# Kernel optimization log

Measured on AMD Instinct MI355X. Metric: run time of the kernel, lower is better.

## Reference

```python
import jax, jax.numpy as jnp
import numpy as np

N, NFEAT, NHID1, NHID2, NCLASS, ATT_H = 6000, 512, 64, 64, 8, 16
ALPHA = 0.2
NEG_INF = -9e15


def _xavier(key, shape, gain=1.414):
    fan_in, fan_out = shape[0], shape[1]
    a = gain * np.sqrt(6.0 / (fan_in + fan_out))
    return jax.random.uniform(key, shape, jnp.float32, -a, a)


def setup_inputs() -> dict:
    key = jax.random.key(0)
    ks = jax.random.split(key, 24)
    inp = {
        'x': jax.random.normal(ks[0], (N, NFEAT), jnp.float32),
        'sadj': jax.random.randint(ks[1], (N, N), 0, 2, jnp.int32),
        'fadj': jax.random.randint(ks[2], (N, N), 0, 2, jnp.int32),
    }
    i = 3
    for pfx in ('s1', 's2', 'c'):
        inp[pfx + '_w1'] = _xavier(ks[i], (NFEAT, NHID1)); i += 1
        inp[pfx + '_a1'] = _xavier(ks[i], (2 * NHID1, 1)); i += 1
        inp[pfx + '_w2'] = _xavier(ks[i], (NHID1, NHID2)); i += 1
        inp[pfx + '_a2'] = _xavier(ks[i], (2 * NHID2, 1)); i += 1
    inp['att_w1'] = _xavier(ks[i], (NHID2, ATT_H), 1.0); i += 1
    inp['att_b1'] = jnp.zeros((ATT_H,), jnp.float32)
    inp['att_w2'] = _xavier(ks[i], (ATT_H, 1), 1.0); i += 1
    inp['mlp_w'] = _xavier(ks[i], (NHID2, NCLASS), 1.0); i += 1
    inp['mlp_b'] = jnp.zeros((NCLASS,), jnp.float32)
    return inp


def gat_layer(h, adj, w, a, concat):
    # h: [N, F_in], adj: [N, N] (0/1), w: [F_in, F_out], a: [2*F_out, 1]
    d = w.shape[1]
    Wh = h @ w                               # [N, F_out]
    e = (Wh @ a[:d]) + (Wh @ a[d:]).T        # [N,1] + [1,N] -> [N,N]
    e = jax.nn.leaky_relu(e, ALPHA)
    att = jnp.where(adj > 0, e, NEG_INF)
    att = jax.nn.softmax(att, axis=1)        # masked row softmax (dropout=0 in eval)
    h_prime = att @ Wh                       # [N, F_out]
    return jax.nn.elu(h_prime) if concat else h_prime


def gat_net(x, adj, w1, a1, w2, a2):
    # nheads=1: single head concat == head output
    h = gat_layer(x, adj, w1, a1, concat=True)
    h = jax.nn.elu(gat_layer(h, adj, w2, a2, concat=False))
    return jax.nn.log_softmax(h, axis=1)


def reference(x, sadj, fadj,
              s1_w1, s1_a1, s1_w2, s1_a2,
              s2_w1, s2_a1, s2_w2, s2_a2,
              c_w1, c_a1, c_w2, c_a2,
              att_w1, att_b1, att_w2, mlp_w, mlp_b):
    emb1 = gat_net(x, sadj, s1_w1, s1_a1, s1_w2, s1_a2)
    com1 = gat_net(x, sadj, c_w1, c_a1, c_w2, c_a2)
    com2 = gat_net(x, fadj, c_w1, c_a1, c_w2, c_a2)
    emb2 = gat_net(x, fadj, s2_w1, s2_a1, s2_w2, s2_a2)
    Xcom = (com1 + com2) / 2
    z = jnp.stack([emb1, emb2, Xcom], axis=1)        # [N, 3, nhid2]
    w = jnp.tanh(z @ att_w1 + att_b1) @ att_w2       # [N, 3, 1]
    beta = jax.nn.softmax(w, axis=1)
    emb = (beta * z).sum(axis=1)                     # [N, nhid2]
    output = jax.nn.log_softmax(emb @ mlp_w + mlp_b, axis=1)
    return (output, beta, emb1, com1, com2, emb2, emb)
```

## Files before the change

kernel.cpp:

```cpp
#include <hip/hip_runtime.h>
#include <cstdint>
#include <cstddef>

#define NN 6000
#define WPR 96
#define NWORDS 94
#define LOG2E 1.4426950408889634f

#define OFF_OUTPUT 0
#define OFF_BETA   48000
#define OFF_EMB1   66000
#define OFF_COM1   450000
#define OFF_COM2   834000
#define OFF_EMB2   1218000
#define OFF_EMB    1602000

typedef unsigned long long u64;
typedef unsigned int uint;
typedef unsigned short ushort;

typedef __bf16 bf16x8 __attribute__((ext_vector_type(8)));
typedef float f32x4 __attribute__((ext_vector_type(4)));
typedef ushort u16x8 __attribute__((ext_vector_type(8)));

__device__ __forceinline__ float wsum64(float v) {
#pragma unroll
  for (int off = 32; off > 0; off >>= 1) v += __shfl_xor(v, off);
  return v;
}

__device__ __forceinline__ ushort bf16rne(float x) {
  uint b = __float_as_uint(x);
  uint r = b + 0x7FFFu + ((b >> 16) & 1u);
  return (ushort)(r >> 16);
}
__device__ __forceinline__ float bf16tof(ushort h) {
  return __uint_as_float((uint)h << 16);
}

__global__ __launch_bounds__(256) void pack_kernel(const int* __restrict__ sadj,
                                                   const int* __restrict__ fadj,
                                                   u64* __restrict__ sbits,
                                                   u64* __restrict__ fbits) {
  const int lane = threadIdx.x & 63;
  const int wid = (blockIdx.x * 256 + threadIdx.x) >> 6;
  const int nw = (gridDim.x * 256) >> 6;
  const int per_mat = NN * WPR;
  for (int t = wid; t < 2 * per_mat; t += nw) {
    int m = t / per_mat;
    int rem = t - m * per_mat;
    int row = rem / WPR;
    int wi = rem - row * WPR;
    const int* adj = m ? fadj : sadj;
    int j = wi * 64 + lane;
    int pred = 0;
    if (j < NN) pred = (adj[(size_t)row * NN + j] != 0);
    u64 mask = __ballot(pred);
    if (lane == 0) (m ? fbits : sbits)[row * WPR + wi] = mask;
  }
}

struct GemmArgs { const float* X; const float* W; const float* A; float* wh; float* f; float* g; };
struct GemmArgs4 { GemmArgs a[4]; };

__global__ __launch_bounds__(256) void gemm_fg_kernel(GemmArgs4 P, int K) {
  GemmArgs A = P.a[blockIdx.y];
  const int w = threadIdx.x >> 6, lane = threadIdx.x & 63;
  const int r0 = blockIdx.x * 16 + w * 4;
  float acc[4] = {0.f, 0.f, 0.f, 0.f};
  const float* X0 = A.X + (size_t)r0 * K;
  for (int k = 0; k < K; k += 4) {
    float xa[4][4];
    *(float4*)xa[0] = *(const float4*)(X0 + k);
    *(float4*)xa[1] = *(const float4*)(X0 + K + k);
    *(float4*)xa[2] = *(const float4*)(X0 + 2 * (size_t)K + k);
    *(float4*)xa[3] = *(const float4*)(X0 + 3 * (size_t)K + k);
#pragma unroll
    for (int kk = 0; kk < 4; ++kk) {
      float wv = A.W[(size_t)(k + kk) * 64 + lane];
#pragma unroll
      for (int r = 0; r < 4; ++r) acc[r] = fmaf(xa[r][kk], wv, acc[r]);
    }
  }
  float af = A.A[lane], ag = A.A[64 + lane];
#pragma unroll
  for (int r = 0; r < 4; ++r) {
    A.wh[(size_t)(r0 + r) * 64 + lane] = acc[r];
    float pf = wsum64(acc[r] * af);
    float pg = wsum64(acc[r] * ag);
    if (lane == 0) { A.f[r0 + r] = pf * LOG2E; A.g[r0 + r] = pg * LOG2E; }
  }
}

struct TransArgs { const float* wh; ushort* bhi; ushort* blo; };
struct TransArgs4 { TransArgs a[4]; };

__global__ __launch_bounds__(256) void trans_kernel(TransArgs4 P) {
  TransArgs A = P.a[blockIdx.y];
  const int jt = blockIdx.x;
  __shared__ float t[64][69];
  const int tid = threadIdx.x;
#pragma unroll
  for (int it = 0; it < 4; ++it) {
    int jl = (tid >> 4) + it * 16;
    int j = jt * 64 + jl;
    float4 v = make_float4(0.f, 0.f, 0.f, 0.f);
    if (j < NN) v = *(const float4*)(A.wh + (size_t)j * 64 + (tid & 15) * 4);
    int d0 = (tid & 15) * 4;
    t[jl][d0] = v.x; t[jl][d0 + 1] = v.y; t[jl][d0 + 2] = v.z; t[jl][d0 + 3] = v.w;
  }
  __syncthreads();
  const int w = tid >> 6, lane = tid & 63, q = lane >> 4, m16 = lane & 15;
#pragma unroll
  for (int fi0 = 0; fi0 < 2; ++fi0) {
    int fi = w + fi0 * 4;
    int k0 = fi >> 2, n0 = fi & 3;
    u16x8 hv, lv;
#pragma unroll
    for (int i = 0; i < 8; ++i) {
      float x = t[k0 * 32 + q * 8 + i][n0 * 16 + m16];
      ushort h = bf16rne(x);
      hv[i] = h;
      lv[i] = bf16rne(x - bf16tof(h));
    }
    size_t off = ((size_t)jt * 8 + fi) * 64 + lane;
    *(u16x8*)(A.bhi + off * 8) = hv;
    *(u16x8*)(A.blo + off * 8) = lv;
  }
}

struct Agg2Args { const u64* bits; const float* f; const float* g;
                  const ushort* bhi; const ushort* blo; float* out; };
struct Agg2Args4 { Agg2Args a[4]; };

template <int MODE>
__global__ __launch_bounds__(512) void agg2_kernel(Agg2Args4 P) {
  const int bid = blockIdx.x;
  const int combo = (bid & 7) >> 1;
  const int mt = ((bid >> 3) << 1) | (bid & 1);
  Agg2Args A = P.a[combo];
  const int w = threadIdx.x >> 6, lane = threadIdx.x & 63;
  const int rg = w & 3, jh = w >> 2;
  const int q = lane >> 4, m16 = lane & 15;
  const int row = mt * 64 + rg * 16 + m16;
  const int rc = row < NN ? row : NN - 1;
  const float fr = A.f[rc];
  const u64* brow = A.bits + (size_t)rc * WPR;

  f32x4 acc[4] = {{0,0,0,0},{0,0,0,0},{0,0,0,0},{0,0,0,0}};
  float sp = 0.f;

  for (int jt = jh; jt < NWORDS; jt += 2) {
    u64 word = brow[jt];
    u16x8 ph[2], pl[2];
#pragma unroll
    for (int k0 = 0; k0 < 2; ++k0) {
      uint byt = (uint)(word >> (k0 * 32 + q * 8)) & 0xFFu;
      const float* gp = A.g + jt * 64 + k0 * 32 + q * 8;
      float4 gA = *(const float4*)gp;
      float4 gB = *(const float4*)(gp + 4);
      float ge[8] = {gA.x, gA.y, gA.z, gA.w, gB.x, gB.y, gB.z, gB.w};
      u16x8 hv, lv;
#pragma unroll
      for (int i = 0; i < 8; ++i) {
        float e = fr + ge[i];
        float lr = fmaxf(e, 0.2f * e);
        float p = exp2f(lr);
        p = (byt & (1u << i)) ? p : 0.f;
        sp += p;
        ushort h = bf16rne(p);
        hv[i] = h;
        lv[i] = bf16rne(p - bf16tof(h));
      }
      ph[k0] = hv; pl[k0] = lv;
    }
    const u16x8* BH = (const u16x8*)A.bhi + ((size_t)jt * 8) * 64 + lane;
    const u16x8* BL = (const u16x8*)A.blo + ((size_t)jt * 8) * 64 + lane;
    bf16x8 a0h = __builtin_bit_cast(bf16x8, ph[0]);
    bf16x8 a1h = __builtin_bit_cast(bf16x8, ph[1]);
    bf16x8 a0l = __builtin_bit_cast(bf16x8, pl[0]);
    bf16x8 a1l = __builtin_bit_cast(bf16x8, pl[1]);
#pragma unroll
    for (int n0 = 0; n0 < 4; ++n0) {
      u16x8 bh0 = BH[n0 * 64], bh1 = BH[(4 + n0) * 64];
      u16x8 bl0 = BL[n0 * 64], bl1 = BL[(4 + n0) * 64];
      bf16x8 b0h = __builtin_bit_cast(bf16x8, bh0);
      bf16x8 b1h = __builtin_bit_cast(bf16x8, bh1);
      bf16x8 b0l = __builtin_bit_cast(bf16x8, bl0);
      bf16x8 b1l = __builtin_bit_cast(bf16x8, bl1);
      acc[n0] = __builtin_amdgcn_mfma_f32_16x16x32_bf16(a0h, b0h, acc[n0], 0, 0, 0);
      acc[n0] = __builtin_amdgcn_mfma_f32_16x16x32_bf16(a1h, b1h, acc[n0], 0, 0, 0);
      acc[n0] = __builtin_amdgcn_mfma_f32_16x16x32_bf16(a0h, b0l, acc[n0], 0, 0, 0);
      acc[n0] = __builtin_amdgcn_mfma_f32_16x16x32_bf16(a1h, b1l, acc[n0], 0, 0, 0);
      acc[n0] = __builtin_amdgcn_mfma_f32_16x16x32_bf16(a0l, b0h, acc[n0], 0, 0, 0);
      acc[n0] = __builtin_amdgcn_mfma_f32_16x16x32_bf16(a1l, b1h, acc[n0], 0, 0, 0);
    }
  }

  sp += __shfl_xor(sp, 16);
  sp += __shfl_xor(sp, 32);

  __shared__ float cb[64][68];
  __shared__ float spb[64];
  if (jh == 0) {
#pragma unroll
    for (int n0 = 0; n0 < 4; ++n0)
#pragma unroll
      for (int r = 0; r < 4; ++r)
        cb[rg * 16 + q * 4 + r][n0 * 16 + m16] = acc[n0][r];
    if (lane < 16) spb[rg * 16 + lane] = sp;
  }
  __syncthreads();
  if (jh == 1) {
    if (lane < 16) spb[rg * 16 + lane] += sp;
  }
  __syncthreads();
  if (jh == 1) {
    float ot[4][4];
#pragma unroll
    for (int r = 0; r < 4; ++r) {
      float sprow = spb[rg * 16 + q * 4 + r];
#pragma unroll
      for (int n0 = 0; n0 < 4; ++n0) {
        float o = acc[n0][r] + cb[rg * 16 + q * 4 + r][n0 * 16 + m16];
        o /= sprow;
        ot[n0][r] = (o > 0.f) ? o : expm1f(o);
      }
    }
#pragma unroll
    for (int r = 0; r < 4; ++r) {
      int orow = mt * 64 + rg * 16 + q * 4 + r;
      float v0 = ot[0][r], v1 = ot[1][r], v2 = ot[2][r], v3 = ot[3][r];
      if (MODE == 1) {
        float mx = fmaxf(fmaxf(v0, v1), fmaxf(v2, v3));
#pragma unroll
        for (int off = 1; off < 16; off <<= 1) mx = fmaxf(mx, __shfl_xor(mx, off));
        float se = __expf(v0 - mx) + __expf(v1 - mx) + __expf(v2 - mx) + __expf(v3 - mx);
#pragma unroll
        for (int off = 1; off < 16; off <<= 1) se += __shfl_xor(se, off);
        float lse = mx + logf(se);
        v0 -= lse; v1 -= lse; v2 -= lse; v3 -= lse;
      }
      if (orow < NN) {
        float* op = A.out + (size_t)orow * 64 + m16;
        op[0] = v0; op[16] = v1; op[32] = v2; op[48] = v3;
      }
    }
  }
}

__global__ __launch_bounds__(256) void fuse_kernel(float* __restrict__ out,
                                                   const float* __restrict__ aw1,
                                                   const float* __restrict__ ab1,
                                                   const float* __restrict__ aw2,
                                                   const float* __restrict__ mlpw,
                                                   const float* __restrict__ mlpb) {
  __shared__ float zs[4][64];
  const int w = threadIdx.x >> 6, lane = threadIdx.x & 63;
  const int i = blockIdx.x * 4 + w;

  const float* emb1 = out + OFF_EMB1;
  const float* com1 = out + OFF_COM1;
  const float* com2 = out + OFF_COM2;
  const float* emb2 = out + OFF_EMB2;

  float z0 = emb1[(size_t)i * 64 + lane];
  float z1 = emb2[(size_t)i * 64 + lane];
  float z2 = 0.5f * (com1[(size_t)i * 64 + lane] + com2[(size_t)i * 64 + lane]);
  float zk[3] = {z0, z1, z2};
  float wk[3];
#pragma unroll
  for (int k = 0; k < 3; ++k) {
    zs[w][lane] = zk[k];
    int h = lane & 15;
    float dot = ab1[h];
    for (int d = 0; d < 64; ++d) dot = fmaf(zs[w][d], aw1[d * 16 + h], dot);
    float c = tanhf(dot) * aw2[h];
#pragma unroll
    for (int off = 1; off < 16; off <<= 1) c += __shfl_xor(c, off);
    wk[k] = c;
  }
  float mw = fmaxf(wk[0], fmaxf(wk[1], wk[2]));
  float e0 = __expf(wk[0] - mw), e1 = __expf(wk[1] - mw), e2 = __expf(wk[2] - mw);
  float s = e0 + e1 + e2;
  float b0 = e0 / s, b1 = e1 / s, b2 = e2 / s;
  float emb = b0 * z0 + b1 * z1 + b2 * z2;
  out[OFF_EMB + (size_t)i * 64 + lane] = emb;
  if (lane == 0) {
    float* bp = out + OFF_BETA + (size_t)i * 3;
    bp[0] = b0; bp[1] = b1; bp[2] = b2;
  }
  zs[w][lane] = emb;
  int c8 = lane & 7;
  float lg = mlpb[c8];
  for (int d = 0; d < 64; ++d) lg = fmaf(zs[w][d], mlpw[d * 8 + c8], lg);
  float mx = lg;
#pragma unroll
  for (int off = 1; off < 8; off <<= 1) mx = fmaxf(mx, __shfl_xor(mx, off));
  float ex = __expf(lg - mx);
  float se = ex;
#pragma unroll
  for (int off = 1; off < 8; off <<= 1) se += __shfl_xor(se, off);
  float res = lg - mx - logf(se);
  if (lane < 8) out[OFF_OUTPUT + (size_t)i * 8 + lane] = res;
}

extern "C" void kernel_launch(void* const* d_in, const int* in_sizes, int n_in,
                              void* d_out, int out_size, void* d_ws, size_t ws_size,
                              hipStream_t stream) {
  const float* x   = (const float*)d_in[0];
  const int* sadj  = (const int*)d_in[1];
  const int* fadj  = (const int*)d_in[2];
  const float* w1[3] = {(const float*)d_in[3], (const float*)d_in[7], (const float*)d_in[11]};
  const float* a1[3] = {(const float*)d_in[4], (const float*)d_in[8], (const float*)d_in[12]};
  const float* w2[3] = {(const float*)d_in[5], (const float*)d_in[9], (const float*)d_in[13]};
  const float* a2[3] = {(const float*)d_in[6], (const float*)d_in[10], (const float*)d_in[14]};
  const float* aw1  = (const float*)d_in[15];
  const float* ab1  = (const float*)d_in[16];
  const float* aw2  = (const float*)d_in[17];
  const float* mlpw = (const float*)d_in[18];
  const float* mlpb = (const float*)d_in[19];
  float* out = (float*)d_out;

  char* p = (char*)d_ws;
  auto alloc = [&](size_t bytes) { char* r = p; p += (bytes + 255) & ~(size_t)255; return r; };
  const size_t FRAG_ELEMS = (size_t)NWORDS * 8 * 64 * 8;
  u64* sbits = (u64*)alloc((size_t)NN * WPR * 8);
  u64* fbits = (u64*)alloc((size_t)NN * WPR * 8);
  float *Wh1[3], *f1[3], *g1[3];
  ushort *hi1[3], *lo1[3];
  for (int n = 0; n < 3; ++n) Wh1[n] = (float*)alloc((size_t)NN * 64 * 4);
  for (int n = 0; n < 3; ++n) f1[n] = (float*)alloc(6144 * 4);
  for (int n = 0; n < 3; ++n) g1[n] = (float*)alloc(6144 * 4);
  for (int n = 0; n < 3; ++n) { hi1[n] = (ushort*)alloc(FRAG_ELEMS * 2); lo1[n] = (ushort*)alloc(FRAG_ELEMS * 2); }
  float *h1[4], *Wh2[4], *f2[4], *g2[4];
  ushort *hi2[4], *lo2[4];
  for (int c = 0; c < 4; ++c) h1[c] = (float*)alloc((size_t)NN * 64 * 4);
  for (int c = 0; c < 4; ++c) Wh2[c] = (float*)alloc((size_t)NN * 64 * 4);
  for (int c = 0; c < 4; ++c) f2[c] = (float*)alloc(6144 * 4);
  for (int c = 0; c < 4; ++c) g2[c] = (float*)alloc(6144 * 4);
  for (int c = 0; c < 4; ++c) { hi2[c] = (ushort*)alloc(FRAG_ELEMS * 2); lo2[c] = (ushort*)alloc(FRAG_ELEMS * 2); }

  const int cn[4] = {0, 2, 2, 1};
  const u64* cb[4] = {sbits, sbits, fbits, fbits};
  float* cout[4] = {out + OFF_EMB1, out + OFF_COM1, out + OFF_COM2, out + OFF_EMB2};

  pack_kernel<<<dim3(2048), dim3(256), 0, stream>>>(sadj, fadj, sbits, fbits);

  GemmArgs4 ga1;
  for (int n = 0; n < 3; ++n) ga1.a[n] = {x, w1[n], a1[n], Wh1[n], f1[n], g1[n]};
  ga1.a[3] = ga1.a[0];
  gemm_fg_kernel<<<dim3(375, 3), dim3(256), 0, stream>>>(ga1, 512);

  TransArgs4 ta1;
  for (int n = 0; n < 3; ++n) ta1.a[n] = {Wh1[n], hi1[n], lo1[n]};
  ta1.a[3] = ta1.a[0];
  trans_kernel<<<dim3(NWORDS, 3), dim3(256), 0, stream>>>(ta1);

  Agg2Args4 aa1;
  for (int c = 0; c < 4; ++c) aa1.a[c] = {cb[c], f1[cn[c]], g1[cn[c]], hi1[cn[c]], lo1[cn[c]], h1[c]};
  agg2_kernel<0><<<dim3(376), dim3(512), 0, stream>>>(aa1);

  GemmArgs4 ga2;
  for (int c = 0; c < 4; ++c) ga2.a[c] = {h1[c], w2[cn[c]], a2[cn[c]], Wh2[c], f2[c], g2[c]};
  gemm_fg_kernel<<<dim3(375, 4), dim3(256), 0, stream>>>(ga2, 64);

  TransArgs4 ta2;
  for (int c = 0; c < 4; ++c) ta2.a[c] = {Wh2[c], hi2[c], lo2[c]};
  trans_kernel<<<dim3(NWORDS, 4), dim3(256), 0, stream>>>(ta2);

  Agg2Args4 aa2;
  for (int c = 0; c < 4; ++c) aa2.a[c] = {cb[c], f2[c], g2[c], hi2[c], lo2[c], cout[c]};
  agg2_kernel<1><<<dim3(376), dim3(512), 0, stream>>>(aa2);

  fuse_kernel<<<dim3(1500), dim3(256), 0, stream>>>(out, aw1, ab1, aw2, mlpw, mlpb);
}
```

Baseline: 832.2 us.

## Pack adjacency rows with wide loads and stage GEMM X tiles in LDS

The pack kernel now gives one wavefront per adjacency row. Each lane reads eight ints with two int4 loads and writes one packed byte, replacing the per-element ballot loop with its integer divisions. The GEMM kernel copies the block's 16 rows of X into shared memory once and reads from LDS, instead of each wave issuing strided global loads. Byte-wise packing relies on little-endian bit order matching the earlier ballot layout. The 32KB LDS tile may reduce occupancy.

Result: faster. 745.9 us (-10.4%).

```diff
diff --git a/kernel.cpp b/kernel.cpp
--- a/kernel.cpp
+++ b/kernel.cpp
@@ -18,6 +18,7 @@
 typedef unsigned long long u64;
 typedef unsigned int uint;
 typedef unsigned short ushort;
+typedef unsigned char uchar;
 
 typedef __bf16 bf16x8 __attribute__((ext_vector_type(8)));
 typedef float f32x4 __attribute__((ext_vector_type(4)));
@@ -44,19 +45,23 @@
                                                    u64* __restrict__ fbits) {
   const int lane = threadIdx.x & 63;
   const int wid = (blockIdx.x * 256 + threadIdx.x) >> 6;
-  const int nw = (gridDim.x * 256) >> 6;
-  const int per_mat = NN * WPR;
-  for (int t = wid; t < 2 * per_mat; t += nw) {
-    int m = t / per_mat;
-    int rem = t - m * per_mat;
-    int row = rem / WPR;
-    int wi = rem - row * WPR;
-    const int* adj = m ? fadj : sadj;
-    int j = wi * 64 + lane;
-    int pred = 0;
-    if (j < NN) pred = (adj[(size_t)row * NN + j] != 0);
-    u64 mask = __ballot(pred);
-    if (lane == 0) (m ? fbits : sbits)[row * WPR + wi] = mask;
+  const int m = wid >= NN;
+  const int row = m ? wid - NN : wid;
+  const int* arow = (m ? fadj : sadj) + (size_t)row * NN;
+  uchar* brow = (uchar*)(m ? fbits : sbits) + (size_t)row * (WPR * 8);
+#pragma unroll
+  for (int it = 0; it < 12; ++it) {
+    int byte = it * 64 + lane;
+    uint b = 0;
+    if (byte < 750) {
+      const int4* p4 = (const int4*)(arow + byte * 8);
+      int4 v0 = p4[0], v1 = p4[1];
+      b = (uint)(v0.x != 0) | ((uint)(v0.y != 0) << 1) |
+          ((uint)(v0.z != 0) << 2) | ((uint)(v0.w != 0) << 3) |
+          ((uint)(v1.x != 0) << 4) | ((uint)(v1.y != 0) << 5) |
+          ((uint)(v1.z != 0) << 6) | ((uint)(v1.w != 0) << 7);
+    }
+    brow[byte] = (uchar)b;
   }
 }
 
@@ -65,16 +70,24 @@
 
 __global__ __launch_bounds__(256) void gemm_fg_kernel(GemmArgs4 P, int K) {
   GemmArgs A = P.a[blockIdx.y];
-  const int w = threadIdx.x >> 6, lane = threadIdx.x & 63;
-  const int r0 = blockIdx.x * 16 + w * 4;
+  __shared__ float xs[16 * 512];
+  const int tid = threadIdx.x;
+  const int w = tid >> 6, lane = tid & 63;
+  const int r0b = blockIdx.x * 16;
+  const float* Xb = A.X + (size_t)r0b * K;
+  const int nf4 = (16 * K) >> 2;
+  for (int i = tid; i < nf4; i += 256)
+    *(float4*)&xs[i * 4] = *(const float4*)(Xb + (size_t)i * 4);
+  __syncthreads();
+
+  const int r0 = w * 4;
   float acc[4] = {0.f, 0.f, 0.f, 0.f};
-  const float* X0 = A.X + (size_t)r0 * K;
   for (int k = 0; k < K; k += 4) {
     float xa[4][4];
-    *(float4*)xa[0] = *(const float4*)(X0 + k);
-    *(float4*)xa[1] = *(const float4*)(X0 + K + k);
-    *(float4*)xa[2] = *(const float4*)(X0 + 2 * (size_t)K + k);
-    *(float4*)xa[3] = *(const float4*)(X0 + 3 * (size_t)K + k);
+    *(float4*)xa[0] = *(const float4*)&xs[(r0 + 0) * K + k];
+    *(float4*)xa[1] = *(const float4*)&xs[(r0 + 1) * K + k];
+    *(float4*)xa[2] = *(const float4*)&xs[(r0 + 2) * K + k];
+    *(float4*)xa[3] = *(const float4*)&xs[(r0 + 3) * K + k];
 #pragma unroll
     for (int kk = 0; kk < 4; ++kk) {
       float wv = A.W[(size_t)(k + kk) * 64 + lane];
@@ -85,10 +98,10 @@
   float af = A.A[lane], ag = A.A[64 + lane];
 #pragma unroll
   for (int r = 0; r < 4; ++r) {
-    A.wh[(size_t)(r0 + r) * 64 + lane] = acc[r];
+    A.wh[(size_t)(r0b + r0 + r) * 64 + lane] = acc[r];
     float pf = wsum64(acc[r] * af);
     float pg = wsum64(acc[r] * ag);
-    if (lane == 0) { A.f[r0 + r] = pf * LOG2E; A.g[r0 + r] = pg * LOG2E; }
+    if (lane == 0) { A.f[r0b + r0 + r] = pf * LOG2E; A.g[r0b + r0 + r] = pg * LOG2E; }
   }
 }
 
@@ -345,7 +358,7 @@
   const u64* cb[4] = {sbits, sbits, fbits, fbits};
   float* cout[4] = {out + OFF_EMB1, out + OFF_COM1, out + OFF_COM2, out + OFF_EMB2};
 
-  pack_kernel<<<dim3(2048), dim3(256), 0, stream>>>(sadj, fadj, sbits, fbits);
+  pack_kernel<<<dim3(3000), dim3(256), 0, stream>>>(sadj, fadj, sbits, fbits);
 
   GemmArgs4 ga1;
   for (int n = 0; n < 3; ++n) ga1.a[n] = {x, w1[n], a1[n], Wh1[n], f1[n], g1[n]};
```
